# Performance work log

Hardware: AMD Instinct MI355X
Metric: run time of the kernel (lower is better)

The kernel has to match this reference:

```python
import jax, jax.numpy as jnp
import numpy as np

B, D, O = 256, 4096, 16384


def setup_inputs() -> dict:
    key = jax.random.key(0)
    k1, k2, k3, k4 = jax.random.split(key, 4)
    x1 = jax.random.normal(k1, (B, D), dtype=jnp.float32)
    x2 = jax.random.normal(k2, (B, D), dtype=jnp.float32)
    # random hash buckets in [0, O) and random +/-1 signs (homogeneous: shared by both inputs)
    h1 = jax.random.randint(k3, (D,), 0, O, dtype=jnp.int32)
    s1 = jnp.where(jax.random.uniform(k4, (D,)) < 0.5, -1.0, 1.0).astype(jnp.float32)
    return {"x1": x1, "x2": x2, "h1": h1, "s1": s1, "output_size": O}


def reference(x1, x2, h1, s1, output_size):
    # psi(): count-sketch via sign-multiply + scatter-add along feature axis
    batch = x1.shape[0]
    y1 = jnp.zeros((batch, output_size), x1.dtype).at[:, h1].add(s1 * x1)  # [B, O]
    y2 = jnp.zeros((batch, output_size), x2.dtype).at[:, h1].add(s1 * x2)  # [B, O]
    # conv(): circular convolution of the two sketches via FFT pointwise product
    out = jnp.fft.ifft(jnp.fft.fft(y1, axis=-1) * jnp.fft.fft(y2, axis=-1), axis=-1)
    return out.real.astype(x1.dtype)
```

## Files before the change

### kernel.cpp

```cpp
#include <hip/hip_runtime.h>


#define FFT_N   16384
#define LOGN    14
#define BLOCK   1024
#define DIM     4096
#define SLOT(e) ((e) + ((e) >> 4))
#define LDS_SLOTS 17408

__device__ __forceinline__ float2 cmul(float2 a, float2 b) {
    return make_float2(a.x * b.x - a.y * b.y, a.x * b.y + a.y * b.x);
}
__device__ __forceinline__ float2 csqr(float2 a) {
    return make_float2(a.x * a.x - a.y * a.y, 2.f * a.x * a.y);
}

#define CT0 1.0f
#define DECL_TW_TABLES \
    const float CT[8] = {1.f, 0.92387953f, 0.70710678f, 0.38268343f, 0.f, -0.38268343f, -0.70710678f, -0.92387953f}; \
    const float ST[8] = {0.f, 0.38268343f, 0.70710678f, 0.92387953f, 1.f, 0.92387953f, 0.70710678f, 0.38268343f};

template<int PMAX>
__device__ __forceinline__ void fft16_dif(float2* r, float phi) {
    DECL_TW_TABLES
    float2 W[4];
    if (PMAX == 3) {
        __sincosf(phi, &W[3].y, &W[3].x);
        W[2] = csqr(W[3]); W[1] = csqr(W[2]); W[0] = csqr(W[1]);
    } else {
        W[0] = W[1] = W[2] = W[3] = make_float2(1.f, 0.f);
    }
    #pragma unroll
    for (int p = PMAX; p >= 0; --p) {
        #pragma unroll
        for (int h = 0; h < 8; ++h) {
            const int jp = h & ((1 << p) - 1);
            const int j  = ((h >> p) << (p + 1)) | jp;
            const int ci = jp << (3 - p);
            const float2 T = cmul(W[p], make_float2(CT[ci], -ST[ci]));
            float2 a = r[j], b = r[j + (1 << p)];
            r[j] = make_float2(a.x + b.x, a.y + b.y);
            float2 d = make_float2(a.x - b.x, a.y - b.y);
            r[j + (1 << p)] = cmul(d, T);
        }
    }
}

template<int PMAX>
__device__ __forceinline__ void fft16_dit(float2* r, float phi) {
    DECL_TW_TABLES
    float2 W[4];
    if (PMAX == 3) {
        __sincosf(phi, &W[3].y, &W[3].x);
        W[2] = csqr(W[3]); W[1] = csqr(W[2]); W[0] = csqr(W[1]);
    } else {
        W[0] = W[1] = W[2] = W[3] = make_float2(1.f, 0.f);
    }
    #pragma unroll
    for (int p = 0; p <= PMAX; ++p) {
        #pragma unroll
        for (int h = 0; h < 8; ++h) {
            const int jp = h & ((1 << p) - 1);
            const int j  = ((h >> p) << (p + 1)) | jp;
            const int ci = jp << (3 - p);
            const float2 T = cmul(W[p], make_float2(CT[ci], ST[ci]));
            float2 a = r[j];
            float2 b = cmul(r[j + (1 << p)], T);
            r[j]            = make_float2(a.x + b.x, a.y + b.y);
            r[j + (1 << p)] = make_float2(a.x - b.x, a.y - b.y);
        }
    }
}

__launch_bounds__(BLOCK)
__global__ void cbp_fft_kernel(const float* __restrict__ x1,
                               const float* __restrict__ x2,
                               const int* __restrict__ h1,
                               const float* __restrict__ s1,
                               float* __restrict__ out) {
    __shared__ float2 zz[LDS_SLOTS];
    const int tid = threadIdx.x;
    const int b   = blockIdx.x;

    #pragma unroll
    for (int i = tid; i < LDS_SLOTS; i += BLOCK) zz[i] = make_float2(0.f, 0.f);
    __syncthreads();

    const float* x1r = x1 + (size_t)b * DIM;
    const float* x2r = x2 + (size_t)b * DIM;
    #pragma unroll
    for (int i = 0; i < DIM / BLOCK; ++i) {
        int d = tid + i * BLOCK;
        float s = s1[d];
        int   h = h1[d];
        atomicAdd(&zz[SLOT(h)].x, s * x1r[d]);
        atomicAdd(&zz[SLOT(h)].y, s * x2r[d]);
    }
    __syncthreads();

    float2 r[16];

    #pragma unroll
    for (int j = 0; j < 16; ++j) r[j] = zz[SLOT(tid + (j << 10))];
    fft16_dif<3>(r, (float)tid * (-3.14159265358979323846f / 8192.f));
    #pragma unroll
    for (int j = 0; j < 16; ++j) zz[SLOT(tid + (j << 10))] = r[j];
    __syncthreads();

    {
        const int base = ((tid >> 6) << 10) | (tid & 63);
        #pragma unroll
        for (int j = 0; j < 16; ++j) r[j] = zz[SLOT(base + (j << 6))];
        fft16_dif<3>(r, (float)(tid & 63) * (-3.14159265358979323846f / 512.f));
        #pragma unroll
        for (int j = 0; j < 16; ++j) zz[SLOT(base + (j << 6))] = r[j];
    }
    __syncthreads();

    {
        const int base = ((tid >> 2) << 6) | (tid & 3);
        #pragma unroll
        for (int j = 0; j < 16; ++j) r[j] = zz[SLOT(base + (j << 2))];
        fft16_dif<3>(r, (float)(tid & 3) * (-3.14159265358979323846f / 32.f));
        #pragma unroll
        for (int j = 0; j < 16; ++j) zz[SLOT(base + (j << 2))] = r[j];
    }
    __syncthreads();

    {
        const int base = tid << 4;
        #pragma unroll
        for (int j = 0; j < 16; ++j) r[j] = zz[SLOT(base + j)];
        fft16_dif<1>(r, 0.f);
        #pragma unroll
        for (int j = 0; j < 16; ++j) zz[SLOT(base + j)] = r[j];
    }
    __syncthreads();

    #pragma unroll
    for (int jj = 0; jj < FFT_N / BLOCK; ++jj) {
        int j  = tid + jj * BLOCK;
        int f  = (int)(__brev((unsigned)j) >> (32 - LOGN));
        int fp = (FFT_N - f) & (FFT_N - 1);
        if (f < fp) {
            int jp = (int)(__brev((unsigned)fp) >> (32 - LOGN));
            float2 a = zz[SLOT(j)];
            float2 c = zz[SLOT(jp)];
            float ar = a.x * a.x - a.y * a.y;
            float cr = c.x * c.x - c.y * c.y;
            float xr = ar - cr;
            float xi = 2.f * (a.x * a.y + c.x * c.y);
            zz[SLOT(j)]  = make_float2(0.25f * xi, -0.25f * xr);
            zz[SLOT(jp)] = make_float2(0.25f * xi,  0.25f * xr);
        } else if (f == fp) {
            float2 a = zz[SLOT(j)];
            zz[SLOT(j)] = make_float2(a.x * a.y, 0.f);
        }
    }
    __syncthreads();

    {
        const int base = tid << 4;
        #pragma unroll
        for (int j = 0; j < 16; ++j) r[j] = zz[SLOT(base + j)];
        fft16_dit<1>(r, 0.f);
        #pragma unroll
        for (int j = 0; j < 16; ++j) zz[SLOT(base + j)] = r[j];
    }
    __syncthreads();

    {
        const int base = ((tid >> 2) << 6) | (tid & 3);
        #pragma unroll
        for (int j = 0; j < 16; ++j) r[j] = zz[SLOT(base + (j << 2))];
        fft16_dit<3>(r, (float)(tid & 3) * (3.14159265358979323846f / 32.f));
        #pragma unroll
        for (int j = 0; j < 16; ++j) zz[SLOT(base + (j << 2))] = r[j];
    }
    __syncthreads();

    {
        const int base = ((tid >> 6) << 10) | (tid & 63);
        #pragma unroll
        for (int j = 0; j < 16; ++j) r[j] = zz[SLOT(base + (j << 6))];
        fft16_dit<3>(r, (float)(tid & 63) * (3.14159265358979323846f / 512.f));
        #pragma unroll
        for (int j = 0; j < 16; ++j) zz[SLOT(base + (j << 6))] = r[j];
    }
    __syncthreads();

    #pragma unroll
    for (int j = 0; j < 16; ++j) r[j] = zz[SLOT(tid + (j << 10))];
    fft16_dit<3>(r, (float)tid * (3.14159265358979323846f / 8192.f));

    float* outr = out + (size_t)b * FFT_N;
    const float inv_n = 1.0f / (float)FFT_N;
    #pragma unroll
    for (int j = 0; j < 16; ++j) {
        outr[tid + (j << 10)] = r[j].x * inv_n;
    }
}

extern "C" void kernel_launch(void* const* d_in, const int* in_sizes, int n_in,
                              void* d_out, int out_size, void* d_ws, size_t ws_size,
                              hipStream_t stream) {
    const float* x1 = (const float*)d_in[0];
    const float* x2 = (const float*)d_in[1];
    const int*   h1 = (const int*)d_in[2];
    const float* s1 = (const float*)d_in[3];
    float* out = (float*)d_out;
    const int B = in_sizes[0] / DIM;
    cbp_fft_kernel<<<B, BLOCK, 0, stream>>>(x1, x2, h1, s1, out);
}
```

Measured before the change: 103.3 us.

## Fuse inner FFT passes per wavefront with DPP radix-4 and XOR-swizzled LDS

Each wavefront owns a contiguous 1024-element segment after the first radix-16 pass, so the second and third passes are merged without a block barrier, using only an lgkmcnt wait. The final radix-4 pass is replaced by cross-lane DPP butterflies (xor1/xor2) instead of an LDS round trip. LDS padding is replaced by an XOR swizzle, which shrinks shared memory and drops the extra zeroing. This removes several __syncthreads and LDS passes in both the forward and inverse transforms. It relies on correct intra-wave ordering and DPP semantics, and it changes the data ordering the pointwise-product stage sees.

After: 109.9 us. +6.3%, slower.

```diff
diff --git a/kernel.cpp b/kernel.cpp
--- a/kernel.cpp
+++ b/kernel.cpp
@@ -5,8 +5,7 @@
 #define LOGN    14
 #define BLOCK   1024
 #define DIM     4096
-#define SLOT(e) ((e) + ((e) >> 4))
-#define LDS_SLOTS 17408
+#define SLOT(e) ((e) ^ (((e) >> 4) & 15))
 
 __device__ __forceinline__ float2 cmul(float2 a, float2 b) {
     return make_float2(a.x * b.x - a.y * b.y, a.x * b.y + a.y * b.x);
@@ -15,23 +14,27 @@
     return make_float2(a.x * a.x - a.y * a.y, 2.f * a.x * a.y);
 }
 
-#define CT0 1.0f
+template<int CTRL>
+__device__ __forceinline__ float2 dpp2(float2 v) {
+    float2 o;
+    o.x = __int_as_float(__builtin_amdgcn_update_dpp(0, __float_as_int(v.x), CTRL, 0xF, 0xF, false));
+    o.y = __int_as_float(__builtin_amdgcn_update_dpp(0, __float_as_int(v.y), CTRL, 0xF, 0xF, false));
+    return o;
+}
+#define DPP_XOR1 0xB1
+#define DPP_XOR2 0x4E
+
 #define DECL_TW_TABLES \
     const float CT[8] = {1.f, 0.92387953f, 0.70710678f, 0.38268343f, 0.f, -0.38268343f, -0.70710678f, -0.92387953f}; \
     const float ST[8] = {0.f, 0.38268343f, 0.70710678f, 0.92387953f, 1.f, 0.92387953f, 0.70710678f, 0.38268343f};
 
-template<int PMAX>
 __device__ __forceinline__ void fft16_dif(float2* r, float phi) {
     DECL_TW_TABLES
     float2 W[4];
-    if (PMAX == 3) {
-        __sincosf(phi, &W[3].y, &W[3].x);
-        W[2] = csqr(W[3]); W[1] = csqr(W[2]); W[0] = csqr(W[1]);
-    } else {
-        W[0] = W[1] = W[2] = W[3] = make_float2(1.f, 0.f);
-    }
-    #pragma unroll
-    for (int p = PMAX; p >= 0; --p) {
+    __sincosf(phi, &W[3].y, &W[3].x);
+    W[2] = csqr(W[3]); W[1] = csqr(W[2]); W[0] = csqr(W[1]);
+    #pragma unroll
+    for (int p = 3; p >= 0; --p) {
         #pragma unroll
         for (int h = 0; h < 8; ++h) {
             const int jp = h & ((1 << p) - 1);
@@ -46,18 +49,13 @@
     }
 }
 
-template<int PMAX>
 __device__ __forceinline__ void fft16_dit(float2* r, float phi) {
     DECL_TW_TABLES
     float2 W[4];
-    if (PMAX == 3) {
-        __sincosf(phi, &W[3].y, &W[3].x);
-        W[2] = csqr(W[3]); W[1] = csqr(W[2]); W[0] = csqr(W[1]);
-    } else {
-        W[0] = W[1] = W[2] = W[3] = make_float2(1.f, 0.f);
-    }
-    #pragma unroll
-    for (int p = 0; p <= PMAX; ++p) {
+    __sincosf(phi, &W[3].y, &W[3].x);
+    W[2] = csqr(W[3]); W[1] = csqr(W[2]); W[0] = csqr(W[1]);
+    #pragma unroll
+    for (int p = 0; p <= 3; ++p) {
         #pragma unroll
         for (int h = 0; h < 8; ++h) {
             const int jp = h & ((1 << p) - 1);
@@ -78,12 +76,14 @@
                                const int* __restrict__ h1,
                                const float* __restrict__ s1,
                                float* __restrict__ out) {
-    __shared__ float2 zz[LDS_SLOTS];
+    __shared__ float2 zz[FFT_N];
     const int tid = threadIdx.x;
+    const int l   = tid & 63;
+    const int w   = tid >> 6;
     const int b   = blockIdx.x;
 
     #pragma unroll
-    for (int i = tid; i < LDS_SLOTS; i += BLOCK) zz[i] = make_float2(0.f, 0.f);
+    for (int j = 0; j < 16; ++j) zz[tid + (j << 10)] = make_float2(0.f, 0.f);
     __syncthreads();
 
     const float* x1r = x1 + (size_t)b * DIM;
@@ -99,42 +99,46 @@
     __syncthreads();
 
     float2 r[16];
+    const int W  = w << 10;
+    const int cb = W + (l & 3) + ((l >> 2) << 6);
 
     #pragma unroll
     for (int j = 0; j < 16; ++j) r[j] = zz[SLOT(tid + (j << 10))];
-    fft16_dif<3>(r, (float)tid * (-3.14159265358979323846f / 8192.f));
+    fft16_dif(r, (float)tid * (-3.14159265358979323846f / 8192.f));
     #pragma unroll
     for (int j = 0; j < 16; ++j) zz[SLOT(tid + (j << 10))] = r[j];
     __syncthreads();
 
+    #pragma unroll
+    for (int j = 0; j < 16; ++j) r[j] = zz[SLOT(W + l + (j << 6))];
+    fft16_dif(r, (float)l * (-3.14159265358979323846f / 512.f));
+    #pragma unroll
+    for (int j = 0; j < 16; ++j) zz[SLOT(W + l + (j << 6))] = r[j];
+    __asm__ volatile("s_waitcnt lgkmcnt(0)" ::: "memory");
+    #pragma unroll
+    for (int j = 0; j < 16; ++j) r[j] = zz[SLOT(cb + (j << 2))];
+    fft16_dif(r, (float)(l & 3) * (-3.14159265358979323846f / 32.f));
     {
-        const int base = ((tid >> 6) << 10) | (tid & 63);
-        #pragma unroll
-        for (int j = 0; j < 16; ++j) r[j] = zz[SLOT(base + (j << 6))];
-        fft16_dif<3>(r, (float)(tid & 63) * (-3.14159265358979323846f / 512.f));
-        #pragma unroll
-        for (int j = 0; j < 16; ++j) zz[SLOT(base + (j << 6))] = r[j];
-    }
-    __syncthreads();
-
-    {
-        const int base = ((tid >> 2) << 6) | (tid & 3);
-        #pragma unroll
-        for (int j = 0; j < 16; ++j) r[j] = zz[SLOT(base + (j << 2))];
-        fft16_dif<3>(r, (float)(tid & 3) * (-3.14159265358979323846f / 32.f));
-        #pragma unroll
-        for (int j = 0; j < 16; ++j) zz[SLOT(base + (j << 2))] = r[j];
-    }
-    __syncthreads();
-
-    {
-        const int base = tid << 4;
-        #pragma unroll
-        for (int j = 0; j < 16; ++j) r[j] = zz[SLOT(base + j)];
-        fft16_dif<1>(r, 0.f);
-        #pragma unroll
-        for (int j = 0; j < 16; ++j) zz[SLOT(base + j)] = r[j];
-    }
+        const float s2  = (l & 2) ? -1.f : 1.f;
+        const bool  hiT = ((l & 3) == 3);
+        #pragma unroll
+        for (int j = 0; j < 16; ++j) {
+            float2 v = dpp2<DPP_XOR2>(r[j]);
+            float dx = fmaf(s2, r[j].x, v.x);
+            float dy = fmaf(s2, r[j].y, v.y);
+            r[j].x = hiT ?  dy : dx;
+            r[j].y = hiT ? -dx : dy;
+        }
+        const float s1v = (l & 1) ? -1.f : 1.f;
+        #pragma unroll
+        for (int j = 0; j < 16; ++j) {
+            float2 v = dpp2<DPP_XOR1>(r[j]);
+            r[j].x = fmaf(s1v, r[j].x, v.x);
+            r[j].y = fmaf(s1v, r[j].y, v.y);
+        }
+    }
+    #pragma unroll
+    for (int j = 0; j < 16; ++j) zz[SLOT(cb + (j << 2))] = r[j];
     __syncthreads();
 
     #pragma unroll
@@ -159,39 +163,43 @@
     }
     __syncthreads();
 
+    #pragma unroll
+    for (int j = 0; j < 16; ++j) r[j] = zz[SLOT(cb + (j << 2))];
     {
-        const int base = tid << 4;
-        #pragma unroll
-        for (int j = 0; j < 16; ++j) r[j] = zz[SLOT(base + j)];
-        fft16_dit<1>(r, 0.f);
-        #pragma unroll
-        for (int j = 0; j < 16; ++j) zz[SLOT(base + j)] = r[j];
-    }
-    __syncthreads();
-
-    {
-        const int base = ((tid >> 2) << 6) | (tid & 3);
-        #pragma unroll
-        for (int j = 0; j < 16; ++j) r[j] = zz[SLOT(base + (j << 2))];
-        fft16_dit<3>(r, (float)(tid & 3) * (3.14159265358979323846f / 32.f));
-        #pragma unroll
-        for (int j = 0; j < 16; ++j) zz[SLOT(base + (j << 2))] = r[j];
-    }
-    __syncthreads();
-
-    {
-        const int base = ((tid >> 6) << 10) | (tid & 63);
-        #pragma unroll
-        for (int j = 0; j < 16; ++j) r[j] = zz[SLOT(base + (j << 6))];
-        fft16_dit<3>(r, (float)(tid & 63) * (3.14159265358979323846f / 512.f));
-        #pragma unroll
-        for (int j = 0; j < 16; ++j) zz[SLOT(base + (j << 6))] = r[j];
-    }
+        const float s1v = (l & 1) ? -1.f : 1.f;
+        #pragma unroll
+        for (int j = 0; j < 16; ++j) {
+            float2 v = dpp2<DPP_XOR1>(r[j]);
+            r[j].x = fmaf(s1v, r[j].x, v.x);
+            r[j].y = fmaf(s1v, r[j].y, v.y);
+        }
+        const float s2  = (l & 2) ? -1.f : 1.f;
+        const bool  hiT = ((l & 3) == 3);
+        #pragma unroll
+        for (int j = 0; j < 16; ++j) {
+            float2 x = r[j];
+            float xr = hiT ? -x.y : x.x;
+            float xi = hiT ?  x.x : x.y;
+            x.x = xr; x.y = xi;
+            float2 v = dpp2<DPP_XOR2>(x);
+            r[j].x = fmaf(s2, x.x, v.x);
+            r[j].y = fmaf(s2, x.y, v.y);
+        }
+    }
+    fft16_dit(r, (float)(l & 3) * (3.14159265358979323846f / 32.f));
+    #pragma unroll
+    for (int j = 0; j < 16; ++j) zz[SLOT(cb + (j << 2))] = r[j];
+    __asm__ volatile("s_waitcnt lgkmcnt(0)" ::: "memory");
+    #pragma unroll
+    for (int j = 0; j < 16; ++j) r[j] = zz[SLOT(W + l + (j << 6))];
+    fft16_dit(r, (float)l * (3.14159265358979323846f / 512.f));
+    #pragma unroll
+    for (int j = 0; j < 16; ++j) zz[SLOT(W + l + (j << 6))] = r[j];
     __syncthreads();
 
     #pragma unroll
     for (int j = 0; j < 16; ++j) r[j] = zz[SLOT(tid + (j << 10))];
-    fft16_dit<3>(r, (float)tid * (3.14159265358979323846f / 8192.f));
+    fft16_dit(r, (float)tid * (3.14159265358979323846f / 8192.f));
 
     float* outr = out + (size_t)b * FFT_N;
     const float inv_n = 1.0f / (float)FFT_N;
```

## Restructure FFT into radix-8 passes with XOR swizzle and wave-local fences

Applied to the files above, without the earlier changes.

Replaces the four radix-16 passes with four radix-8 passes plus a radix-4 pass, with each thread handling two or four sub-FFTs per pass. The two innermost passes on each side of the pointwise product use only an LDS wait fence instead of a block barrier, because their data stays within one wavefront's slice. It also changes the bank-conflict padding to an XOR swizzle so LDS shrinks to exactly FFT_N float2, and raises the launch-bounds occupancy hint. The aim is fewer block barriers and lower register pressure, in exchange for more LDS round trips.

After: 100.1 us. -3.1%, faster.

```diff
diff --git a/kernel.cpp b/kernel.cpp
--- a/kernel.cpp
+++ b/kernel.cpp
@@ -5,8 +5,8 @@
 #define LOGN    14
 #define BLOCK   1024
 #define DIM     4096
-#define SLOT(e) ((e) + ((e) >> 4))
-#define LDS_SLOTS 17408
+#define SLOT(e) ((e) ^ (((e) >> 4) & 15))
+#define PI_F    3.14159265358979323846f
 
 __device__ __forceinline__ float2 cmul(float2 a, float2 b) {
     return make_float2(a.x * b.x - a.y * b.y, a.x * b.y + a.y * b.x);
@@ -15,29 +15,20 @@
     return make_float2(a.x * a.x - a.y * a.y, 2.f * a.x * a.y);
 }
 
-#define CT0 1.0f
-#define DECL_TW_TABLES \
-    const float CT[8] = {1.f, 0.92387953f, 0.70710678f, 0.38268343f, 0.f, -0.38268343f, -0.70710678f, -0.92387953f}; \
-    const float ST[8] = {0.f, 0.38268343f, 0.70710678f, 0.92387953f, 1.f, 0.92387953f, 0.70710678f, 0.38268343f};
-
-template<int PMAX>
-__device__ __forceinline__ void fft16_dif(float2* r, float phi) {
-    DECL_TW_TABLES
-    float2 W[4];
-    if (PMAX == 3) {
-        __sincosf(phi, &W[3].y, &W[3].x);
-        W[2] = csqr(W[3]); W[1] = csqr(W[2]); W[0] = csqr(W[1]);
-    } else {
-        W[0] = W[1] = W[2] = W[3] = make_float2(1.f, 0.f);
-    }
-    #pragma unroll
-    for (int p = PMAX; p >= 0; --p) {
-        #pragma unroll
-        for (int h = 0; h < 8; ++h) {
+__device__ __forceinline__ void fft8_dif(float2* r, float phi) {
+    const float CT8[4] = {1.f, 0.70710678f, 0.f, -0.70710678f};
+    const float ST8[4] = {0.f, 0.70710678f, 1.f, 0.70710678f};
+    float2 W[3];
+    __sincosf(phi, &W[2].y, &W[2].x);
+    W[1] = csqr(W[2]); W[0] = csqr(W[1]);
+    #pragma unroll
+    for (int p = 2; p >= 0; --p) {
+        #pragma unroll
+        for (int h = 0; h < 4; ++h) {
             const int jp = h & ((1 << p) - 1);
             const int j  = ((h >> p) << (p + 1)) | jp;
-            const int ci = jp << (3 - p);
-            const float2 T = cmul(W[p], make_float2(CT[ci], -ST[ci]));
+            const int ci = jp << (2 - p);
+            const float2 T = cmul(W[p], make_float2(CT8[ci], -ST8[ci]));
             float2 a = r[j], b = r[j + (1 << p)];
             r[j] = make_float2(a.x + b.x, a.y + b.y);
             float2 d = make_float2(a.x - b.x, a.y - b.y);
@@ -46,24 +37,20 @@
     }
 }
 
-template<int PMAX>
-__device__ __forceinline__ void fft16_dit(float2* r, float phi) {
-    DECL_TW_TABLES
-    float2 W[4];
-    if (PMAX == 3) {
-        __sincosf(phi, &W[3].y, &W[3].x);
-        W[2] = csqr(W[3]); W[1] = csqr(W[2]); W[0] = csqr(W[1]);
-    } else {
-        W[0] = W[1] = W[2] = W[3] = make_float2(1.f, 0.f);
-    }
-    #pragma unroll
-    for (int p = 0; p <= PMAX; ++p) {
-        #pragma unroll
-        for (int h = 0; h < 8; ++h) {
+__device__ __forceinline__ void fft8_dit(float2* r, float phi) {
+    const float CT8[4] = {1.f, 0.70710678f, 0.f, -0.70710678f};
+    const float ST8[4] = {0.f, 0.70710678f, 1.f, 0.70710678f};
+    float2 W[3];
+    __sincosf(phi, &W[2].y, &W[2].x);
+    W[1] = csqr(W[2]); W[0] = csqr(W[1]);
+    #pragma unroll
+    for (int p = 0; p <= 2; ++p) {
+        #pragma unroll
+        for (int h = 0; h < 4; ++h) {
             const int jp = h & ((1 << p) - 1);
             const int j  = ((h >> p) << (p + 1)) | jp;
-            const int ci = jp << (3 - p);
-            const float2 T = cmul(W[p], make_float2(CT[ci], ST[ci]));
+            const int ci = jp << (2 - p);
+            const float2 T = cmul(W[p], make_float2(CT8[ci], ST8[ci]));
             float2 a = r[j];
             float2 b = cmul(r[j + (1 << p)], T);
             r[j]            = make_float2(a.x + b.x, a.y + b.y);
@@ -72,18 +59,63 @@
     }
 }
 
-__launch_bounds__(BLOCK)
+__device__ __forceinline__ void fft4_dif(float2* r) {
+    float2 a, b, d;
+    a = r[0]; b = r[2]; r[0] = make_float2(a.x + b.x, a.y + b.y);
+    r[2] = make_float2(a.x - b.x, a.y - b.y);
+    a = r[1]; b = r[3]; r[1] = make_float2(a.x + b.x, a.y + b.y);
+    d = make_float2(a.x - b.x, a.y - b.y);
+    r[3] = make_float2(d.y, -d.x);
+    a = r[0]; b = r[1]; r[0] = make_float2(a.x + b.x, a.y + b.y);
+    r[1] = make_float2(a.x - b.x, a.y - b.y);
+    a = r[2]; b = r[3]; r[2] = make_float2(a.x + b.x, a.y + b.y);
+    r[3] = make_float2(a.x - b.x, a.y - b.y);
+}
+
+__device__ __forceinline__ void fft4_dit(float2* r) {
+    float2 a, b;
+    a = r[0]; b = r[1]; r[0] = make_float2(a.x + b.x, a.y + b.y);
+    r[1] = make_float2(a.x - b.x, a.y - b.y);
+    a = r[2]; b = r[3]; r[2] = make_float2(a.x + b.x, a.y + b.y);
+    r[3] = make_float2(a.x - b.x, a.y - b.y);
+    a = r[0]; b = r[2]; r[0] = make_float2(a.x + b.x, a.y + b.y);
+    r[2] = make_float2(a.x - b.x, a.y - b.y);
+    a = r[1]; b = make_float2(-r[3].y, r[3].x);
+    r[1] = make_float2(a.x + b.x, a.y + b.y);
+    r[3] = make_float2(a.x - b.x, a.y - b.y);
+}
+
+__device__ __forceinline__ void pass8_dif(float2* zz, int base, int slog, float phi) {
+    float2 r[8];
+    #pragma unroll
+    for (int j = 0; j < 8; ++j) r[j] = zz[SLOT(base + (j << slog))];
+    fft8_dif(r, phi);
+    #pragma unroll
+    for (int j = 0; j < 8; ++j) zz[SLOT(base + (j << slog))] = r[j];
+}
+__device__ __forceinline__ void pass8_dit(float2* zz, int base, int slog, float phi) {
+    float2 r[8];
+    #pragma unroll
+    for (int j = 0; j < 8; ++j) r[j] = zz[SLOT(base + (j << slog))];
+    fft8_dit(r, phi);
+    #pragma unroll
+    for (int j = 0; j < 8; ++j) zz[SLOT(base + (j << slog))] = r[j];
+}
+
+#define WAVE_FENCE() __asm__ volatile("s_waitcnt lgkmcnt(0)" ::: "memory")
+
+__launch_bounds__(BLOCK, 4)
 __global__ void cbp_fft_kernel(const float* __restrict__ x1,
                                const float* __restrict__ x2,
                                const int* __restrict__ h1,
                                const float* __restrict__ s1,
                                float* __restrict__ out) {
-    __shared__ float2 zz[LDS_SLOTS];
+    __shared__ float2 zz[FFT_N];
     const int tid = threadIdx.x;
     const int b   = blockIdx.x;
 
     #pragma unroll
-    for (int i = tid; i < LDS_SLOTS; i += BLOCK) zz[i] = make_float2(0.f, 0.f);
+    for (int j = 0; j < 16; ++j) zz[tid + (j << 10)] = make_float2(0.f, 0.f);
     __syncthreads();
 
     const float* x1r = x1 + (size_t)b * DIM;
@@ -98,42 +130,46 @@
     }
     __syncthreads();
 
-    float2 r[16];
-
-    #pragma unroll
-    for (int j = 0; j < 16; ++j) r[j] = zz[SLOT(tid + (j << 10))];
-    fft16_dif<3>(r, (float)tid * (-3.14159265358979323846f / 8192.f));
-    #pragma unroll
-    for (int j = 0; j < 16; ++j) zz[SLOT(tid + (j << 10))] = r[j];
-    __syncthreads();
-
-    {
-        const int base = ((tid >> 6) << 10) | (tid & 63);
-        #pragma unroll
-        for (int j = 0; j < 16; ++j) r[j] = zz[SLOT(base + (j << 6))];
-        fft16_dif<3>(r, (float)(tid & 63) * (-3.14159265358979323846f / 512.f));
-        #pragma unroll
-        for (int j = 0; j < 16; ++j) zz[SLOT(base + (j << 6))] = r[j];
-    }
-    __syncthreads();
-
-    {
-        const int base = ((tid >> 2) << 6) | (tid & 3);
-        #pragma unroll
-        for (int j = 0; j < 16; ++j) r[j] = zz[SLOT(base + (j << 2))];
-        fft16_dif<3>(r, (float)(tid & 3) * (-3.14159265358979323846f / 32.f));
-        #pragma unroll
-        for (int j = 0; j < 16; ++j) zz[SLOT(base + (j << 2))] = r[j];
-    }
-    __syncthreads();
-
-    {
-        const int base = tid << 4;
-        #pragma unroll
-        for (int j = 0; j < 16; ++j) r[j] = zz[SLOT(base + j)];
-        fft16_dif<1>(r, 0.f);
-        #pragma unroll
-        for (int j = 0; j < 16; ++j) zz[SLOT(base + j)] = r[j];
+    #pragma unroll 1
+    for (int q = 0; q < 2; ++q) {
+        int k = tid + (q << 10);
+        pass8_dif(zz, k, 11, (float)k * (-PI_F / 8192.f));
+    }
+    __syncthreads();
+
+    #pragma unroll 1
+    for (int q = 0; q < 2; ++q) {
+        int g = tid >> 7;
+        int k = (tid & 127) + (q << 7);
+        pass8_dif(zz, (g << 11) + k, 8, (float)k * (-PI_F / 1024.f));
+    }
+    __syncthreads();
+
+    #pragma unroll 1
+    for (int q = 0; q < 2; ++q) {
+        int g = tid >> 4;
+        int k = (tid & 15) + (q << 4);
+        pass8_dif(zz, (g << 8) + k, 5, (float)k * (-PI_F / 128.f));
+    }
+    WAVE_FENCE();
+
+    #pragma unroll 1
+    for (int q = 0; q < 2; ++q) {
+        int g = tid >> 1;
+        int k = (tid & 1) + (q << 1);
+        pass8_dif(zz, (g << 5) + k, 2, (float)k * (-PI_F / 16.f));
+    }
+    WAVE_FENCE();
+
+    #pragma unroll 1
+    for (int q = 0; q < 4; ++q) {
+        int base = (tid << 4) + (q << 2);
+        float2 r[4];
+        #pragma unroll
+        for (int j = 0; j < 4; ++j) r[j] = zz[SLOT(base + j)];
+        fft4_dif(r);
+        #pragma unroll
+        for (int j = 0; j < 4; ++j) zz[SLOT(base + j)] = r[j];
     }
     __syncthreads();
 
@@ -159,45 +195,53 @@
     }
     __syncthreads();
 
-    {
-        const int base = tid << 4;
-        #pragma unroll
-        for (int j = 0; j < 16; ++j) r[j] = zz[SLOT(base + j)];
-        fft16_dit<1>(r, 0.f);
-        #pragma unroll
-        for (int j = 0; j < 16; ++j) zz[SLOT(base + j)] = r[j];
-    }
-    __syncthreads();
-
-    {
-        const int base = ((tid >> 2) << 6) | (tid & 3);
-        #pragma unroll
-        for (int j = 0; j < 16; ++j) r[j] = zz[SLOT(base + (j << 2))];
-        fft16_dit<3>(r, (float)(tid & 3) * (3.14159265358979323846f / 32.f));
-        #pragma unroll
-        for (int j = 0; j < 16; ++j) zz[SLOT(base + (j << 2))] = r[j];
-    }
-    __syncthreads();
-
-    {
-        const int base = ((tid >> 6) << 10) | (tid & 63);
-        #pragma unroll
-        for (int j = 0; j < 16; ++j) r[j] = zz[SLOT(base + (j << 6))];
-        fft16_dit<3>(r, (float)(tid & 63) * (3.14159265358979323846f / 512.f));
-        #pragma unroll
-        for (int j = 0; j < 16; ++j) zz[SLOT(base + (j << 6))] = r[j];
-    }
-    __syncthreads();
-
-    #pragma unroll
-    for (int j = 0; j < 16; ++j) r[j] = zz[SLOT(tid + (j << 10))];
-    fft16_dit<3>(r, (float)tid * (3.14159265358979323846f / 8192.f));
+    #pragma unroll 1
+    for (int q = 0; q < 4; ++q) {
+        int base = (tid << 4) + (q << 2);
+        float2 r[4];
+        #pragma unroll
+        for (int j = 0; j < 4; ++j) r[j] = zz[SLOT(base + j)];
+        fft4_dit(r);
+        #pragma unroll
+        for (int j = 0; j < 4; ++j) zz[SLOT(base + j)] = r[j];
+    }
+    WAVE_FENCE();
+
+    #pragma unroll 1
+    for (int q = 0; q < 2; ++q) {
+        int g = tid >> 1;
+        int k = (tid & 1) + (q << 1);
+        pass8_dit(zz, (g << 5) + k, 2, (float)k * (PI_F / 16.f));
+    }
+    WAVE_FENCE();
+
+    #pragma unroll 1
+    for (int q = 0; q < 2; ++q) {
+        int g = tid >> 4;
+        int k = (tid & 15) + (q << 4);
+        pass8_dit(zz, (g << 8) + k, 5, (float)k * (PI_F / 128.f));
+    }
+    __syncthreads();
+
+    #pragma unroll 1
+    for (int q = 0; q < 2; ++q) {
+        int g = tid >> 7;
+        int k = (tid & 127) + (q << 7);
+        pass8_dit(zz, (g << 11) + k, 8, (float)k * (PI_F / 1024.f));
+    }
+    __syncthreads();
 
     float* outr = out + (size_t)b * FFT_N;
     const float inv_n = 1.0f / (float)FFT_N;
-    #pragma unroll
-    for (int j = 0; j < 16; ++j) {
-        outr[tid + (j << 10)] = r[j].x * inv_n;
+    #pragma unroll 1
+    for (int q = 0; q < 2; ++q) {
+        int k = tid + (q << 10);
+        float2 r[8];
+        #pragma unroll
+        for (int j = 0; j < 8; ++j) r[j] = zz[SLOT(k + (j << 11))];
+        fft8_dit(r, (float)k * (PI_F / 8192.f));
+        #pragma unroll
+        for (int j = 0; j < 8; ++j) outr[k + (j << 11)] = r[j].x * inv_n;
     }
 }
 
```
